# Optimization experiments

Measured on AMD Instinct MI355X. Metric: run time of the kernel, lower is better.

## Reference

```python
import jax, jax.numpy as jnp
import numpy as np

N_NODES = 100000
N_EDGES = 1600000
HID = 128
N_GRAPHS = 512
MAX_Z = 1000
NODE_VOCAB = 200000
OUT = 2
BN_EPS = 1e-5


def setup_inputs() -> dict:
    key = jax.random.key(0)
    ks = jax.random.split(key, 20)

    def w(k, shape, fan_in):
        return jax.random.normal(k, shape, dtype=jnp.float32) / np.sqrt(fan_in)

    inp = {
        "num_nodes": N_NODES,
        "z": jax.random.randint(ks[0], (N_NODES,), 0, MAX_Z),
        "edge_index": jax.random.randint(ks[1], (2, N_EDGES), 0, N_NODES),
        "batch": jnp.sort(jax.random.randint(ks[2], (N_NODES,), 0, N_GRAPHS)),
        "node_id": jax.random.randint(ks[3], (N_NODES,), 0, NODE_VOCAB),
        # parameters
        "z_emb": jax.random.normal(ks[4], (MAX_Z, HID), dtype=jnp.float32) * 0.02,
        "node_emb": jax.random.normal(ks[5], (NODE_VOCAB, HID), dtype=jnp.float32) * 0.02,
        "W0": w(ks[6], (2 * HID, HID), 2 * HID), "b0": jnp.zeros((HID,), jnp.float32),
        "W1": w(ks[7], (HID, HID), HID), "b1": jnp.zeros((HID,), jnp.float32),
        "W2": w(ks[8], (HID, HID), HID), "b2": jnp.zeros((HID,), jnp.float32),
        "mlp_W1": w(ks[9], (HID, HID), HID), "mlp_b1": jnp.zeros((HID,), jnp.float32),
        "bn_gamma": jnp.ones((HID,), jnp.float32), "bn_beta": jnp.zeros((HID,), jnp.float32),
        "mlp_W2": w(ks[10], (HID, OUT), HID), "mlp_b2": jnp.zeros((OUT,), jnp.float32),
    }
    return inp


def _gin_conv(x, src, dst, W, b, num_nodes):
    # GINConv(eps=0): out_i = Linear(x_i + sum_{j->i} x_j)
    agg = jax.ops.segment_sum(x[src], dst, num_segments=num_nodes)
    return (x + agg) @ W + b


def reference(num_nodes, z, edge_index, batch, node_id,
              z_emb, node_emb, W0, b0, W1, b1, W2, b2,
              mlp_W1, mlp_b1, bn_gamma, bn_beta, mlp_W2, mlp_b2):
    src, dst = edge_index[0], edge_index[1]
    # node features: concat(z_embedding(z), node_embedding(node_id)) -> [N, 2H]
    x = jnp.concatenate([z_emb[z], node_emb[node_id]], axis=1)

    x = jax.nn.relu(_gin_conv(x, src, dst, W0, b0, num_nodes))  # [N, H]
    x = jax.nn.relu(_gin_conv(x, src, dst, W1, b1, num_nodes))
    x = _gin_conv(x, src, dst, W2, b2, num_nodes)  # last conv: no relu

    # global mean pool over graphs
    sums = jax.ops.segment_sum(x, batch, num_segments=N_GRAPHS)  # [G, H]
    counts = jax.ops.segment_sum(jnp.ones((num_nodes,), x.dtype), batch,
                                 num_segments=N_GRAPHS)
    pooled = sums / jnp.maximum(counts, 1.0)[:, None]

    # MLP([H, H, OUT]): Linear -> BatchNorm(eval, identity stats) -> ReLU -> Linear
    h = pooled @ mlp_W1 + mlp_b1
    h = h * (bn_gamma / np.sqrt(1.0 + BN_EPS)) + bn_beta
    h = jax.nn.relu(h)
    return h @ mlp_W2 + mlp_b2  # [G, OUT]
```

## Files before the change

### kernel.cpp

```cpp
#include <hip/hip_runtime.h>

#define NN 100000
#define NE 1600000
#define HID 128
#define NG 512
#define MAXZ 1000
#define NBK 256
#define BK_S 391
#define TILE_E 4096

typedef unsigned short u16;
typedef unsigned int u32;
typedef __attribute__((ext_vector_type(8))) short bf16x8;
typedef __attribute__((ext_vector_type(4))) float f32x4;

__device__ __forceinline__ u16 bf16r(float x) {
    u32 u = __float_as_uint(x);
    u32 r = (u + 0x7fffu + ((u >> 16) & 1u)) >> 16;
    return (u16)r;
}
__device__ __forceinline__ float bflo(u32 u) { return __uint_as_float(u << 16); }
__device__ __forceinline__ float bfhi(u32 u) { return __uint_as_float(u & 0xffff0000u); }

__global__ __launch_bounds__(256) void bucket_count_kernel(const int* __restrict__ dst,
                                                           int* __restrict__ bcount) {
    __shared__ int lh[NBK];
    int t = threadIdx.x;
    lh[t] = 0;
    __syncthreads();
    int stride = gridDim.x * 256;
    for (int i = blockIdx.x * 256 + t; i < NE; i += stride)
        atomicAdd(&lh[dst[i] / BK_S], 1);
    __syncthreads();
    int v = lh[t];
    if (v) atomicAdd(&bcount[t], v);
}

__global__ __launch_bounds__(NBK) void scan_nbk_kernel(const int* __restrict__ bcount,
                                                       int* __restrict__ boff,
                                                       int* __restrict__ gcursor) {
    __shared__ int buf[NBK];
    int t = threadIdx.x;
    int v = bcount[t];
    buf[t] = v;
    __syncthreads();
    for (int d = 1; d < NBK; d <<= 1) {
        int add = (t >= d) ? buf[t - d] : 0;
        __syncthreads();
        buf[t] += add;
        __syncthreads();
    }
    int excl = buf[t] - v;
    boff[t] = excl;
    gcursor[t] = excl;
    if (t == NBK - 1) boff[NBK] = buf[NBK - 1];
}

__global__ __launch_bounds__(256) void pair_scatter_kernel(const int* __restrict__ src,
                                                           const int* __restrict__ dst,
                                                           int* __restrict__ gcursor,
                                                           u32* __restrict__ pairs) {
    __shared__ int cnt[NBK];
    __shared__ int base[NBK];
    int t = threadIdx.x;
    long tile0 = (long)blockIdx.x * TILE_E;
    cnt[t] = 0;
    __syncthreads();
    u32 val[16], br[16];
#pragma unroll
    for (int i = 0; i < 16; ++i) {
        long idx = tile0 + i * 256 + t;
        val[i] = 0xFFFFFFFFu;
        if (idx < NE) {
            int d = dst[idx];
            int b = d / BK_S;
            int r = atomicAdd(&cnt[b], 1);
            val[i] = ((u32)(d - b * BK_S) << 17) | (u32)src[idx];
            br[i] = ((u32)b << 12) | (u32)r;
        }
    }
    __syncthreads();
    int c = cnt[t];
    if (c) base[t] = atomicAdd(&gcursor[t], c);
    __syncthreads();
#pragma unroll
    for (int i = 0; i < 16; ++i) {
        if (val[i] != 0xFFFFFFFFu) {
            u32 b = br[i] >> 12, r = br[i] & 0xFFFu;
            pairs[base[b] + r] = val[i];
        }
    }
}

__global__ __launch_bounds__(256) void bucket_build_kernel(const u32* __restrict__ pairs,
                                                           const int* __restrict__ boff,
                                                           int* __restrict__ off,
                                                           int* __restrict__ csr) {
    __shared__ int lh[BK_S];
    __shared__ int ts[256];
    int b = blockIdx.x, t = threadIdx.x;
    int base = boff[b], end = boff[b + 1];
    int node0 = b * BK_S;
    for (int i = t; i < BK_S; i += 256) lh[i] = 0;
    __syncthreads();
    for (int j = base + t; j < end; j += 256)
        atomicAdd(&lh[pairs[j] >> 17], 1);
    __syncthreads();
    int i0 = t * 2, i1 = t * 2 + 1;
    int c0 = (i0 < BK_S) ? lh[i0] : 0;
    int c1 = (i1 < BK_S) ? lh[i1] : 0;
    int s = c0 + c1;
    ts[t] = s;
    __syncthreads();
    for (int d = 1; d < 256; d <<= 1) {
        int add = (t >= d) ? ts[t - d] : 0;
        __syncthreads();
        ts[t] += add;
        __syncthreads();
    }
    int e0 = base + ts[t] - s;
    int e1 = e0 + c0;
    if (i0 < BK_S) { lh[i0] = e0; int n = node0 + i0; if (n < NN) off[n] = e0; }
    if (i1 < BK_S) { lh[i1] = e1; int n = node0 + i1; if (n < NN) off[n] = e1; }
    if (b == 0 && t == 0) off[NN] = NE;
    __syncthreads();
    for (int j = base + t; j < end; j += 256) {
        u32 p = pairs[j];
        int pos = atomicAdd(&lh[p >> 17], 1);
        csr[pos] = (int)(p & 0x1FFFFu);
    }
}

__global__ __launch_bounds__(128) void wt_kernel(const float* __restrict__ W, u16* __restrict__ Wt) {
    int k = blockIdx.x, n = threadIdx.x;
    Wt[n * HID + k] = bf16r(W[k * HID + n]);
}

#define FMA4(acc, s, w) { acc.x += (s)*(w).x; acc.y += (s)*(w).y; acc.z += (s)*(w).z; acc.w += (s)*(w).w; }
__global__ __launch_bounds__(256) void gemm128_kernel(
    const float* __restrict__ X, const float* __restrict__ W,
    float* __restrict__ Y, int nrows)
{
    __shared__ float xs[32][132];
    int t = threadIdx.x;
    int row0 = blockIdx.x * 32;
    int sr = t >> 5;
    int sk = (t & 31) * 4;
#pragma unroll
    for (int p = 0; p < 4; ++p) {
        int r = p * 8 + sr;
        int grow = row0 + r;
        float4 v = make_float4(0.f, 0.f, 0.f, 0.f);
        if (grow < nrows) v = *(const float4*)(X + (long)grow * HID + sk);
        *(float4*)(&xs[r][sk]) = v;
    }
    __syncthreads();
    int cg = t & 31, rg = t >> 5;
    int c = cg * 4, r = rg * 4;
    float4 a0 = make_float4(0,0,0,0), a1 = a0, a2 = a0, a3 = a0;
    for (int k = 0; k < 128; k += 4) {
        float x0[4], x1[4], x2[4], x3[4];
        *(float4*)x0 = *(const float4*)&xs[r + 0][k];
        *(float4*)x1 = *(const float4*)&xs[r + 1][k];
        *(float4*)x2 = *(const float4*)&xs[r + 2][k];
        *(float4*)x3 = *(const float4*)&xs[r + 3][k];
#pragma unroll
        for (int j = 0; j < 4; ++j) {
            float4 w = *(const float4*)(W + (k + j) * HID + c);
            FMA4(a0, x0[j], w); FMA4(a1, x1[j], w); FMA4(a2, x2[j], w); FMA4(a3, x3[j], w);
        }
    }
    float4 accs[4] = {a0, a1, a2, a3};
#pragma unroll
    for (int i = 0; i < 4; ++i) {
        int grow = row0 + r + i;
        if (grow < nrows) *(float4*)(Y + (long)grow * HID + c) = accs[i];
    }
}

template<int SRC_BF16>
__global__ __launch_bounds__(256) void mfma_gemm_kernel(
    const void* __restrict__ Xsrc,
    const int* __restrict__ gatherIdx,
    const u16* __restrict__ Wt,
    const float* __restrict__ addTab, const int* __restrict__ addIdx,
    u16* __restrict__ Y, int nrows)
{
    __shared__ u16 Als[64][136];
    __shared__ u16 Wls[128][136];
    int t = threadIdx.x;
    int row0 = blockIdx.x * 64;

#pragma unroll
    for (int p = 0; p < 2; ++p) {
        int n = p * 64 + (t >> 2);
        int k0 = (t & 3) * 32;
        const u16* src = Wt + n * HID + k0;
        uint4 v0 = *(const uint4*)(src);
        uint4 v1 = *(const uint4*)(src + 8);
        uint4 v2 = *(const uint4*)(src + 16);
        uint4 v3 = *(const uint4*)(src + 24);
        *(uint4*)&Wls[n][k0]      = v0;
        *(uint4*)&Wls[n][k0 + 8]  = v1;
        *(uint4*)&Wls[n][k0 + 16] = v2;
        *(uint4*)&Wls[n][k0 + 24] = v3;
    }

    if (SRC_BF16) {
        const u16* X = (const u16*)Xsrc;
#pragma unroll
        for (int p = 0; p < 4; ++p) {
            int r = p * 16 + (t >> 4);
            int k0 = (t & 15) * 8;
            int grow = row0 + r;
            uint4 v = make_uint4(0, 0, 0, 0);
            if (grow < nrows) {
                long srow = gatherIdx ? (long)gatherIdx[grow] : (long)grow;
                v = *(const uint4*)(X + srow * HID + k0);
            }
            *(uint4*)&Als[r][k0] = v;
        }
    } else {
        const float* X = (const float*)Xsrc;
#pragma unroll
        for (int p = 0; p < 8; ++p) {
            int r = p * 8 + (t >> 5);
            int k0 = (t & 31) * 4;
            int grow = row0 + r;
            float4 v = make_float4(0.f, 0.f, 0.f, 0.f);
            if (grow < nrows) {
                long srow = gatherIdx ? (long)gatherIdx[grow] : (long)grow;
                v = *(const float4*)(X + srow * HID + k0);
            }
            ushort4 b;
            b.x = bf16r(v.x); b.y = bf16r(v.y); b.z = bf16r(v.z); b.w = bf16r(v.w);
            *(ushort4*)&Als[r][k0] = b;
        }
    }
    __syncthreads();

    int w = t >> 6, l = t & 63;
    int lr = l & 15, lq = l >> 4;
    f32x4 acc[8];
#pragma unroll
    for (int i = 0; i < 8; ++i) acc[i] = (f32x4){0.f, 0.f, 0.f, 0.f};

#pragma unroll
    for (int kk = 0; kk < 4; ++kk) {
        bf16x8 af = *(const bf16x8*)&Als[w * 16 + lr][kk * 32 + lq * 8];
#pragma unroll
        for (int nt = 0; nt < 8; ++nt) {
            bf16x8 bf = *(const bf16x8*)&Wls[nt * 16 + lr][kk * 32 + lq * 8];
            acc[nt] = __builtin_amdgcn_mfma_f32_16x16x32_bf16(af, bf, acc[nt], 0, 0, 0);
        }
    }

    int orow = row0 + w * 16 + lq * 4;
#pragma unroll
    for (int r = 0; r < 4; ++r) {
        int grow = orow + r;
        if (grow < nrows) {
            const float* ap = addTab ? (addTab + (long)addIdx[grow] * HID) : nullptr;
#pragma unroll
            for (int nt = 0; nt < 8; ++nt) {
                int col = nt * 16 + lr;
                float v = acc[nt][r];
                if (ap) v += ap[col];
                Y[(long)grow * HID + col] = bf16r(v);
            }
        }
    }
}

__global__ __launch_bounds__(256) void aggregate_kernel(
    const u16* __restrict__ H, u16* __restrict__ Xo,
    const int* __restrict__ off, const int* __restrict__ csr,
    const float* __restrict__ bias, int n, int doRelu)
{
    int node = blockIdx.x * 4 + (threadIdx.x >> 6);
    if (node >= n) return;
    int lane = threadIdx.x & 63;
    int g = lane >> 4, fl = lane & 15;
    int s = off[node], e = off[node + 1];

    float acc[8] = {0.f, 0.f, 0.f, 0.f, 0.f, 0.f, 0.f, 0.f};
    int j = s + g;

    for (; j + 4 < e; j += 8) {
        int i0 = csr[j];
        int i1 = csr[j + 4];
        uint4 v0 = *(const uint4*)(H + (long)i0 * HID + fl * 8);
        uint4 v1 = *(const uint4*)(H + (long)i1 * HID + fl * 8);
        acc[0] += bflo(v0.x); acc[1] += bfhi(v0.x);
        acc[2] += bflo(v0.y); acc[3] += bfhi(v0.y);
        acc[4] += bflo(v0.z); acc[5] += bfhi(v0.z);
        acc[6] += bflo(v0.w); acc[7] += bfhi(v0.w);
        acc[0] += bflo(v1.x); acc[1] += bfhi(v1.x);
        acc[2] += bflo(v1.y); acc[3] += bfhi(v1.y);
        acc[4] += bflo(v1.z); acc[5] += bfhi(v1.z);
        acc[6] += bflo(v1.w); acc[7] += bfhi(v1.w);
    }
    if (j < e) {
        int i0 = csr[j];
        uint4 v0 = *(const uint4*)(H + (long)i0 * HID + fl * 8);
        acc[0] += bflo(v0.x); acc[1] += bfhi(v0.x);
        acc[2] += bflo(v0.y); acc[3] += bfhi(v0.y);
        acc[4] += bflo(v0.z); acc[5] += bfhi(v0.z);
        acc[6] += bflo(v0.w); acc[7] += bfhi(v0.w);
    }

#pragma unroll
    for (int i = 0; i < 8; ++i) {
        acc[i] += __shfl_xor(acc[i], 16);
        acc[i] += __shfl_xor(acc[i], 32);
    }

    if (g == 0) {
        uint4 sv = *(const uint4*)(H + (long)node * HID + fl * 8);
        float4 ba = *(const float4*)(bias + fl * 8);
        float4 bb = *(const float4*)(bias + fl * 8 + 4);
        float r[8];
        r[0] = acc[0] + bflo(sv.x) + ba.x;
        r[1] = acc[1] + bfhi(sv.x) + ba.y;
        r[2] = acc[2] + bflo(sv.y) + ba.z;
        r[3] = acc[3] + bfhi(sv.y) + ba.w;
        r[4] = acc[4] + bflo(sv.z) + bb.x;
        r[5] = acc[5] + bfhi(sv.z) + bb.y;
        r[6] = acc[6] + bflo(sv.w) + bb.z;
        r[7] = acc[7] + bfhi(sv.w) + bb.w;
        if (doRelu) {
#pragma unroll
            for (int i = 0; i < 8; ++i) r[i] = fmaxf(r[i], 0.f);
        }
        uint4 ov;
        ov.x = (u32)bf16r(r[0]) | ((u32)bf16r(r[1]) << 16);
        ov.y = (u32)bf16r(r[2]) | ((u32)bf16r(r[3]) << 16);
        ov.z = (u32)bf16r(r[4]) | ((u32)bf16r(r[5]) << 16);
        ov.w = (u32)bf16r(r[6]) | ((u32)bf16r(r[7]) << 16);
        *(uint4*)(Xo + (long)node * HID + fl * 8) = ov;
    }
}

__global__ __launch_bounds__(256) void pool_kernel(const u16* __restrict__ X, const int* __restrict__ batch,
                                                   int n, float* __restrict__ pooled) {
    __shared__ float red[4][HID];
    int g = blockIdx.x;
    int t = threadIdx.x;
    int grp = t >> 4, fl = t & 15;
    int lo = 0, hi = n;
    while (lo < hi) { int m = (lo + hi) >> 1; if (batch[m] < g) lo = m + 1; else hi = m; }
    int s = lo;
    lo = 0; hi = n;
    while (lo < hi) { int m = (lo + hi) >> 1; if (batch[m] < g + 1) lo = m + 1; else hi = m; }
    int e = lo;

    float acc[8] = {0.f, 0.f, 0.f, 0.f, 0.f, 0.f, 0.f, 0.f};
    for (int i = s + grp; i < e; i += 16) {
        uint4 v = *(const uint4*)(X + (long)i * HID + fl * 8);
        acc[0] += bflo(v.x); acc[1] += bfhi(v.x);
        acc[2] += bflo(v.y); acc[3] += bfhi(v.y);
        acc[4] += bflo(v.z); acc[5] += bfhi(v.z);
        acc[6] += bflo(v.w); acc[7] += bfhi(v.w);
    }
#pragma unroll
    for (int i = 0; i < 8; ++i) {
        acc[i] += __shfl_xor(acc[i], 16);
        acc[i] += __shfl_xor(acc[i], 32);
    }
    int w = t >> 6, lane = t & 63;
    if (lane < 16) {
#pragma unroll
        for (int i = 0; i < 8; ++i) red[w][lane * 8 + i] = acc[i];
    }
    __syncthreads();
    if (t < HID) {
        float v = red[0][t] + red[1][t] + red[2][t] + red[3][t];
        float cnt = (float)(e - s);
        pooled[g * HID + t] = v / fmaxf(cnt, 1.f);
    }
}

__global__ __launch_bounds__(128) void mlp_kernel(
    const float* __restrict__ pooled, const float* __restrict__ W1, const float* __restrict__ b1,
    const float* __restrict__ gamma, const float* __restrict__ beta,
    const float* __restrict__ W2, const float* __restrict__ b2, float* __restrict__ out)
{
    int g = blockIdx.x, t = threadIdx.x;
    __shared__ float p[HID];
    __shared__ float red[4];
    p[t] = pooled[g * HID + t];
    __syncthreads();
    float acc = b1[t];
    for (int k = 0; k < HID; ++k) acc += p[k] * W1[k * HID + t];
    const float inv = 1.0f / sqrtf(1.0f + 1e-5f);
    acc = acc * (gamma[t] * inv) + beta[t];
    acc = fmaxf(acc, 0.f);
    float v0 = acc * W2[t * 2 + 0];
    float v1 = acc * W2[t * 2 + 1];
    for (int d = 32; d > 0; d >>= 1) { v0 += __shfl_down(v0, d); v1 += __shfl_down(v1, d); }
    int w = t >> 6, lane = t & 63;
    if (lane == 0) { red[w * 2] = v0; red[w * 2 + 1] = v1; }
    __syncthreads();
    if (t == 0) {
        out[g * 2 + 0] = red[0] + red[2] + b2[0];
        out[g * 2 + 1] = red[1] + red[3] + b2[1];
    }
}

extern "C" void kernel_launch(void* const* d_in, const int* in_sizes, int n_in,
                              void* d_out, int out_size, void* d_ws, size_t ws_size,
                              hipStream_t stream) {
    const int*   z        = (const int*)d_in[1];
    const int*   ei       = (const int*)d_in[2];
    const int*   batch    = (const int*)d_in[3];
    const int*   node_id  = (const int*)d_in[4];
    const float* z_emb    = (const float*)d_in[5];
    const float* node_emb = (const float*)d_in[6];
    const float* W0  = (const float*)d_in[7];
    const float* b0  = (const float*)d_in[8];
    const float* W1  = (const float*)d_in[9];
    const float* b1  = (const float*)d_in[10];
    const float* W2  = (const float*)d_in[11];
    const float* b2  = (const float*)d_in[12];
    const float* mW1 = (const float*)d_in[13];
    const float* mb1 = (const float*)d_in[14];
    const float* gam = (const float*)d_in[15];
    const float* bet = (const float*)d_in[16];
    const float* mW2 = (const float*)d_in[17];
    const float* mb2 = (const float*)d_in[18];
    float* out = (float*)d_out;

    const int* srcArr = ei;
    const int* dstArr = ei + NE;

    char* ws = (char*)d_ws;
    size_t o = 0;
    auto alloc = [&](size_t bytes) { char* p = ws + o; o += (bytes + 255) & ~(size_t)255; return p; };
    u16*   A      = (u16*)alloc((size_t)NN * HID * 2);
    u16*   B      = (u16*)alloc((size_t)NN * HID * 2);
    float* zW     = (float*)alloc((size_t)MAXZ * HID * 4);
    u16*   W0bt   = (u16*)alloc((size_t)HID * HID * 2);
    u16*   W1t    = (u16*)alloc((size_t)HID * HID * 2);
    u16*   W2t    = (u16*)alloc((size_t)HID * HID * 2);
    int*   bcount = (int*)alloc((size_t)NBK * 4);
    int*   boff   = (int*)alloc((size_t)(NBK + 1) * 4);
    int*   gcur   = (int*)alloc((size_t)NBK * 4);
    u32*   pairs  = (u32*)alloc((size_t)NE * 4);
    int*   off    = (int*)alloc((size_t)(NN + 1) * 4);
    int*   csr    = (int*)alloc((size_t)NE * 4);
    float* pooled = (float*)alloc((size_t)NG * HID * 4);
    (void)ws_size;

    hipMemsetAsync(bcount, 0, (size_t)NBK * 4, stream);
    bucket_count_kernel<<<256, 256, 0, stream>>>(dstArr, bcount);
    scan_nbk_kernel<<<1, NBK, 0, stream>>>(bcount, boff, gcur);
    pair_scatter_kernel<<<(NE + TILE_E - 1) / TILE_E, 256, 0, stream>>>(srcArr, dstArr, gcur, pairs);
    bucket_build_kernel<<<NBK, 256, 0, stream>>>(pairs, boff, off, csr);

    wt_kernel<<<HID, HID, 0, stream>>>(W0 + HID * HID, W0bt);
    wt_kernel<<<HID, HID, 0, stream>>>(W1, W1t);
    wt_kernel<<<HID, HID, 0, stream>>>(W2, W2t);

    gemm128_kernel<<<(MAXZ + 31) / 32, 256, 0, stream>>>(z_emb, W0, zW, MAXZ);

    const int GB = (NN + 63) / 64;
    mfma_gemm_kernel<0><<<GB, 256, 0, stream>>>(node_emb, node_id, W0bt, zW, z, B, NN);
    aggregate_kernel<<<NN / 4, 256, 0, stream>>>(B, A, off, csr, b0, NN, 1);
    mfma_gemm_kernel<1><<<GB, 256, 0, stream>>>(A, nullptr, W1t, nullptr, nullptr, B, NN);
    aggregate_kernel<<<NN / 4, 256, 0, stream>>>(B, A, off, csr, b1, NN, 1);
    mfma_gemm_kernel<1><<<GB, 256, 0, stream>>>(A, nullptr, W2t, nullptr, nullptr, B, NN);
    aggregate_kernel<<<NN / 4, 256, 0, stream>>>(B, A, off, csr, b2, NN, 0);

    pool_kernel<<<NG, 256, 0, stream>>>(A, batch, NN, pooled);
    mlp_kernel<<<NG, 128, 0, stream>>>(pooled, mW1, mb1, gam, bet, mW2, mb2, out);
}
```

Baseline: 370.0 us.

## Fuse neighbor aggregation into following MFMA GEMM and read weights directly

Merges the aggregate (sum over neighbors, add self and bias, ReLU) for layers 0 and 1 with the next layer's MFMA GEMM, so aggregated rows are written to LDS instead of a global intermediate and read back. The weight tile is no longer staged in LDS; each wave reads B fragments straight from global/L2. The goal is to remove two kernel launches and the write-then-read round trip of the intermediate buffers. In exchange each block now covers 64 nodes processed 16 per wave in sequence, which lowers parallelism for the latency-bound gather, and the weight reads go through cache rather than LDS.

```diff
diff --git a/kernel.cpp b/kernel.cpp
--- a/kernel.cpp
+++ b/kernel.cpp
@@ -178,67 +178,10 @@
     }
 }
 
-template<int SRC_BF16>
-__global__ __launch_bounds__(256) void mfma_gemm_kernel(
-    const void* __restrict__ Xsrc,
-    const int* __restrict__ gatherIdx,
-    const u16* __restrict__ Wt,
-    const float* __restrict__ addTab, const int* __restrict__ addIdx,
-    u16* __restrict__ Y, int nrows)
+__device__ __forceinline__ void mfma_phase(const u16 (*Als)[136], const u16* __restrict__ Wt,
+                                           const float* __restrict__ addTab, const int* __restrict__ addIdx,
+                                           u16* __restrict__ Y, int row0, int nrows, int t)
 {
-    __shared__ u16 Als[64][136];
-    __shared__ u16 Wls[128][136];
-    int t = threadIdx.x;
-    int row0 = blockIdx.x * 64;
-
-#pragma unroll
-    for (int p = 0; p < 2; ++p) {
-        int n = p * 64 + (t >> 2);
-        int k0 = (t & 3) * 32;
-        const u16* src = Wt + n * HID + k0;
-        uint4 v0 = *(const uint4*)(src);
-        uint4 v1 = *(const uint4*)(src + 8);
-        uint4 v2 = *(const uint4*)(src + 16);
-        uint4 v3 = *(const uint4*)(src + 24);
-        *(uint4*)&Wls[n][k0]      = v0;
-        *(uint4*)&Wls[n][k0 + 8]  = v1;
-        *(uint4*)&Wls[n][k0 + 16] = v2;
-        *(uint4*)&Wls[n][k0 + 24] = v3;
-    }
-
-    if (SRC_BF16) {
-        const u16* X = (const u16*)Xsrc;
-#pragma unroll
-        for (int p = 0; p < 4; ++p) {
-            int r = p * 16 + (t >> 4);
-            int k0 = (t & 15) * 8;
-            int grow = row0 + r;
-            uint4 v = make_uint4(0, 0, 0, 0);
-            if (grow < nrows) {
-                long srow = gatherIdx ? (long)gatherIdx[grow] : (long)grow;
-                v = *(const uint4*)(X + srow * HID + k0);
-            }
-            *(uint4*)&Als[r][k0] = v;
-        }
-    } else {
-        const float* X = (const float*)Xsrc;
-#pragma unroll
-        for (int p = 0; p < 8; ++p) {
-            int r = p * 8 + (t >> 5);
-            int k0 = (t & 31) * 4;
-            int grow = row0 + r;
-            float4 v = make_float4(0.f, 0.f, 0.f, 0.f);
-            if (grow < nrows) {
-                long srow = gatherIdx ? (long)gatherIdx[grow] : (long)grow;
-                v = *(const float4*)(X + srow * HID + k0);
-            }
-            ushort4 b;
-            b.x = bf16r(v.x); b.y = bf16r(v.y); b.z = bf16r(v.z); b.w = bf16r(v.w);
-            *(ushort4*)&Als[r][k0] = b;
-        }
-    }
-    __syncthreads();
-
     int w = t >> 6, l = t & 63;
     int lr = l & 15, lq = l >> 4;
     f32x4 acc[8];
@@ -250,7 +193,7 @@
         bf16x8 af = *(const bf16x8*)&Als[w * 16 + lr][kk * 32 + lq * 8];
 #pragma unroll
         for (int nt = 0; nt < 8; ++nt) {
-            bf16x8 bf = *(const bf16x8*)&Wls[nt * 16 + lr][kk * 32 + lq * 8];
+            bf16x8 bf = *(const bf16x8*)(Wt + (nt * 16 + lr) * HID + kk * 32 + lq * 8);
             acc[nt] = __builtin_amdgcn_mfma_f32_16x16x32_bf16(af, bf, acc[nt], 0, 0, 0);
         }
     }
@@ -270,6 +213,108 @@
             }
         }
     }
+}
+
+__global__ __launch_bounds__(256) void gemm0_kernel(
+    const float* __restrict__ X, const int* __restrict__ gatherIdx,
+    const u16* __restrict__ Wt,
+    const float* __restrict__ addTab, const int* __restrict__ addIdx,
+    u16* __restrict__ Y, int nrows)
+{
+    __shared__ u16 Als[64][136];
+    int t = threadIdx.x;
+    int row0 = blockIdx.x * 64;
+#pragma unroll
+    for (int p = 0; p < 8; ++p) {
+        int r = p * 8 + (t >> 5);
+        int k0 = (t & 31) * 4;
+        int grow = row0 + r;
+        float4 v = make_float4(0.f, 0.f, 0.f, 0.f);
+        if (grow < nrows) {
+            long srow = (long)gatherIdx[grow];
+            v = *(const float4*)(X + srow * HID + k0);
+        }
+        ushort4 b;
+        b.x = bf16r(v.x); b.y = bf16r(v.y); b.z = bf16r(v.z); b.w = bf16r(v.w);
+        *(ushort4*)&Als[r][k0] = b;
+    }
+    __syncthreads();
+    mfma_phase(Als, Wt, addTab, addIdx, Y, row0, nrows, t);
+}
+
+__global__ __launch_bounds__(256) void fused_agg_gemm_kernel(
+    const u16* __restrict__ H,
+    const int* __restrict__ off, const int* __restrict__ csr,
+    const float* __restrict__ bias,
+    const u16* __restrict__ Wt, u16* __restrict__ Y)
+{
+    __shared__ u16 Als[64][136];
+    int t = threadIdx.x;
+    int row0 = blockIdx.x * 64;
+    int w = t >> 6, l = t & 63;
+    int g = l >> 4, fl = l & 15;
+
+    for (int i = 0; i < 16; ++i) {
+        int r = w * 16 + i;
+        int node = row0 + r;
+        float acc[8] = {0.f, 0.f, 0.f, 0.f, 0.f, 0.f, 0.f, 0.f};
+        if (node < NN) {
+            int s = off[node], e = off[node + 1];
+            int j = s + g;
+            for (; j + 4 < e; j += 8) {
+                int i0 = csr[j];
+                int i1 = csr[j + 4];
+                uint4 v0 = *(const uint4*)(H + (long)i0 * HID + fl * 8);
+                uint4 v1 = *(const uint4*)(H + (long)i1 * HID + fl * 8);
+                acc[0] += bflo(v0.x); acc[1] += bfhi(v0.x);
+                acc[2] += bflo(v0.y); acc[3] += bfhi(v0.y);
+                acc[4] += bflo(v0.z); acc[5] += bfhi(v0.z);
+                acc[6] += bflo(v0.w); acc[7] += bfhi(v0.w);
+                acc[0] += bflo(v1.x); acc[1] += bfhi(v1.x);
+                acc[2] += bflo(v1.y); acc[3] += bfhi(v1.y);
+                acc[4] += bflo(v1.z); acc[5] += bfhi(v1.z);
+                acc[6] += bflo(v1.w); acc[7] += bfhi(v1.w);
+            }
+            if (j < e) {
+                int i0 = csr[j];
+                uint4 v0 = *(const uint4*)(H + (long)i0 * HID + fl * 8);
+                acc[0] += bflo(v0.x); acc[1] += bfhi(v0.x);
+                acc[2] += bflo(v0.y); acc[3] += bfhi(v0.y);
+                acc[4] += bflo(v0.z); acc[5] += bfhi(v0.z);
+                acc[6] += bflo(v0.w); acc[7] += bfhi(v0.w);
+            }
+#pragma unroll
+            for (int q = 0; q < 8; ++q) {
+                acc[q] += __shfl_xor(acc[q], 16);
+                acc[q] += __shfl_xor(acc[q], 32);
+            }
+            if (g == 0) {
+                uint4 sv = *(const uint4*)(H + (long)node * HID + fl * 8);
+                float4 ba = *(const float4*)(bias + fl * 8);
+                float4 bb = *(const float4*)(bias + fl * 8 + 4);
+                float rr[8];
+                rr[0] = acc[0] + bflo(sv.x) + ba.x;
+                rr[1] = acc[1] + bfhi(sv.x) + ba.y;
+                rr[2] = acc[2] + bflo(sv.y) + ba.z;
+                rr[3] = acc[3] + bfhi(sv.y) + ba.w;
+                rr[4] = acc[4] + bflo(sv.z) + bb.x;
+                rr[5] = acc[5] + bfhi(sv.z) + bb.y;
+                rr[6] = acc[6] + bflo(sv.w) + bb.z;
+                rr[7] = acc[7] + bfhi(sv.w) + bb.w;
+                uint4 ov;
+                ov.x = (u32)bf16r(fmaxf(rr[0], 0.f)) | ((u32)bf16r(fmaxf(rr[1], 0.f)) << 16);
+                ov.y = (u32)bf16r(fmaxf(rr[2], 0.f)) | ((u32)bf16r(fmaxf(rr[3], 0.f)) << 16);
+                ov.z = (u32)bf16r(fmaxf(rr[4], 0.f)) | ((u32)bf16r(fmaxf(rr[5], 0.f)) << 16);
+                ov.w = (u32)bf16r(fmaxf(rr[6], 0.f)) | ((u32)bf16r(fmaxf(rr[7], 0.f)) << 16);
+                *(uint4*)&Als[r][fl * 8] = ov;
+            }
+        } else if (g == 0) {
+            uint4 z4 = make_uint4(0, 0, 0, 0);
+            *(uint4*)&Als[r][fl * 8] = z4;
+        }
+    }
+    __syncthreads();
+    mfma_phase(Als, Wt, nullptr, nullptr, Y, row0, NN, t);
 }
 
 __global__ __launch_bounds__(256) void aggregate_kernel(
@@ -464,11 +509,9 @@
     gemm128_kernel<<<(MAXZ + 31) / 32, 256, 0, stream>>>(z_emb, W0, zW, MAXZ);
 
     const int GB = (NN + 63) / 64;
-    mfma_gemm_kernel<0><<<GB, 256, 0, stream>>>(node_emb, node_id, W0bt, zW, z, B, NN);
-    aggregate_kernel<<<NN / 4, 256, 0, stream>>>(B, A, off, csr, b0, NN, 1);
-    mfma_gemm_kernel<1><<<GB, 256, 0, stream>>>(A, nullptr, W1t, nullptr, nullptr, B, NN);
-    aggregate_kernel<<<NN / 4, 256, 0, stream>>>(B, A, off, csr, b1, NN, 1);
-    mfma_gemm_kernel<1><<<GB, 256, 0, stream>>>(A, nullptr, W2t, nullptr, nullptr, B, NN);
+    gemm0_kernel<<<GB, 256, 0, stream>>>(node_emb, node_id, W0bt, zW, z, B, NN);
+    fused_agg_gemm_kernel<<<GB, 256, 0, stream>>>(B, off, csr, b0, W1t, A);
+    fused_agg_gemm_kernel<<<GB, 256, 0, stream>>>(A, off, csr, b1, W2t, B);
     aggregate_kernel<<<NN / 4, 256, 0, stream>>>(B, A, off, csr, b2, NN, 0);
 
     pool_kernel<<<NG, 256, 0, stream>>>(A, batch, NN, pooled);
```

Result: slower. 467.1 us (+26.2%).
